# Performance work log

Hardware: AMD Instinct MI355X
Metric: run time of the kernel (lower is better)

The kernel has to match this reference:

```python
import jax, jax.numpy as jnp
import numpy as np

B, HH, WW = 8, 56, 56
N = HH * WW            # 3136 tokens
DIM, NH, SR = 512, 8, 7
HDIM = DIM // 2        # 256
LDIM = DIM - HDIM      # 256
DH = LDIM // NH        # 32
SCALE = DIM ** -0.5
EPS = 1e-5


def _dwconv(x, w):
    # depthwise 3x3, stride 1, SAME (= padding k//2): x [B,C,H,W], w [C,1,3,3]
    return jax.lax.conv_general_dilated(x, w, (1, 1), 'SAME',
                                        feature_group_count=x.shape[1],
                                        dimension_numbers=('NCHW', 'OIHW', 'NCHW'))


def _bn(x, g, b, m, v):
    # inference BatchNorm2d
    s = g * jax.lax.rsqrt(v + EPS)
    return (x - m[None, :, None, None]) * s[None, :, None, None] + b[None, :, None, None]


def _avg_pool(x, k):
    return jax.lax.reduce_window(x, 0.0, jax.lax.add, (1, 1, k, k), (1, 1, k, k), 'VALID') / (k * k)


def _max_pool(x, k):
    return jax.lax.reduce_window(x, -jnp.inf, jax.lax.max, (1, 1, k, k), (1, 1, k, k), 'VALID')


def setup_inputs() -> dict:
    key = jax.random.key(0)
    ks = jax.random.split(key, 32)
    d = {}
    d['x'] = jax.random.normal(ks[0], (B, N, DIM), jnp.float32)
    d['proj_v_w'] = jax.random.normal(ks[1], (LDIM, HDIM), jnp.float32) / np.sqrt(HDIM).astype(np.float32)
    d['conv1_w'] = jax.random.normal(ks[2], (LDIM, 1, 3, 3), jnp.float32) / 3.0
    d['conv2_w'] = jax.random.normal(ks[3], (LDIM, 1, 3, 3), jnp.float32) / 3.0
    d['conv3_w'] = jax.random.normal(ks[4], (HDIM, LDIM, 1, 1), jnp.float32) / np.sqrt(LDIM).astype(np.float32)
    d['conv3_b'] = jax.random.normal(ks[5], (HDIM,), jnp.float32) * 0.1
    d['v_conv_w'] = jax.random.normal(ks[6], (LDIM, 1, 3, 3), jnp.float32) / 3.0
    d['proj_w'] = jax.random.normal(ks[7], (DIM, DIM), jnp.float32) / np.sqrt(DIM).astype(np.float32)
    d['proj_b'] = jax.random.normal(ks[8], (DIM,), jnp.float32) * 0.1
    i = 9
    for pre, c in (('bn1', LDIM), ('bn2', LDIM), ('bn3', HDIM), ('vbn', LDIM)):
        d[pre + '_g'] = jax.random.uniform(ks[i], (c,), jnp.float32, 0.8, 1.2)
        d[pre + '_b'] = jax.random.normal(ks[i + 1], (c,), jnp.float32) * 0.1
        d[pre + '_m'] = jax.random.normal(ks[i + 2], (c,), jnp.float32) * 0.1
        d[pre + '_v'] = jax.random.uniform(ks[i + 3], (c,), jnp.float32, 0.5, 1.5)
        i += 4
    return d


def reference(x, proj_v_w, conv1_w, conv2_w, conv3_w, conv3_b, v_conv_w, proj_w, proj_b,
              bn1_g, bn1_b, bn1_m, bn1_v, bn2_g, bn2_b, bn2_m, bn2_v,
              bn3_g, bn3_b, bn3_m, bn3_v, vbn_g, vbn_b, vbn_m, vbn_v):
    x_high_in = x[..., :HDIM]                       # [B,N,HDIM]
    v = x_high_in @ proj_v_w.T                      # [B,N,LDIM]
    xh = v.reshape(B, HH, WW, LDIM).transpose(0, 3, 1, 2)   # [B,LDIM,H,W]
    xh = _bn(_dwconv(xh, conv1_w), bn1_g, bn1_b, bn1_m, bn1_v)
    q1 = _avg_pool(xh, SR)                          # [B,LDIM,8,8]
    q2 = _max_pool(xh, SR)
    xh = jax.nn.gelu(xh, approximate=False)
    xh = _bn(_dwconv(xh, conv2_w), bn2_g, bn2_b, bn2_m, bn2_v)
    k1 = _avg_pool(xh, SR)
    k2 = _max_pool(xh, SR)
    xh = jax.lax.conv_general_dilated(xh, conv3_w, (1, 1), 'SAME',
                                      dimension_numbers=('NCHW', 'OIHW', 'NCHW')) + conv3_b[None, :, None, None]
    xh = _bn(xh, bn3_g, bn3_b, bn3_m, bn3_v)
    xh = jax.nn.gelu(xh, approximate=False)
    x_high = xh.reshape(B, HDIM, N).transpose(0, 2, 1)      # [B,N,HDIM]

    hq, wq = HH // SR, WW // SR
    nq = hq * wq                                    # 64 pooled tokens

    def heads(t):                                   # [B,LDIM,hq,wq] -> [B,NH,nq,DH]
        return t.reshape(B, NH, DH, nq).transpose(0, 1, 3, 2)

    q = jnp.concatenate([heads(q1), heads(q2)], axis=-1)    # [B,NH,nq,2*DH]
    k = jnp.concatenate([heads(k1), heads(k2)], axis=-1)
    vh = v.reshape(B, N, NH, DH).transpose(0, 2, 1, 3)      # [B,NH,N,DH]

    attn = jnp.einsum('bhqd,bhkd->bhqk', q, k)              # [B,NH,nq,nq]
    attn = attn.reshape(B * NH, nq, hq, wq)
    attn = jax.image.resize(attn, (B * NH, nq, HH, WW), method='bilinear', antialias=False) * SCALE
    attn = attn.reshape(B, NH, nq, N)
    attn = jax.nn.softmax(attn, axis=-1)

    out = jnp.einsum('bhqn,bhnd->bhqd', attn, vh)           # [B,NH,nq,DH]
    out = out.reshape(B, NH, hq, wq, DH).transpose(0, 1, 4, 2, 3).reshape(B, LDIM, hq, wq)
    out = jax.image.resize(out, (B, LDIM, HH, WW), method='bilinear', antialias=False)
    out = _bn(_dwconv(out, v_conv_w), vbn_g, vbn_b, vbn_m, vbn_v)
    x_low = out.reshape(B, LDIM, N).transpose(0, 2, 1)      # [B,N,LDIM]

    y = jnp.concatenate([x_high, x_low], axis=-1) @ proj_w.T + proj_b
    return y
```

## Files before the change

### kernel.cpp

```cpp
#include <hip/hip_runtime.h>
#include <math.h>

#define BB 8
#define HH 56
#define WWD 56
#define NN 3136
#define CC 256
#define DIMM 512
#define NHEAD 8
#define NQ 64
#define EPSF 1e-5f
#define SCALEF 0.04419417382415922f

typedef __attribute__((ext_vector_type(8))) short short8;
typedef __attribute__((ext_vector_type(4))) short short4v;
typedef __attribute__((ext_vector_type(4))) float floatx4;

__device__ __forceinline__ float gelu_f(float x) {
    float z = x * 0.70710678118654752f;
    float a = fabsf(z);
    float t = __builtin_amdgcn_rcpf(1.f + 0.3275911f * a);
    float p = t * (0.254829592f + t * (-0.284496736f + t * (1.421413741f +
              t * (-1.453152027f + t * 1.061405429f))));
    float e = exp2f(-1.44269504f * a * a);
    float erfa = 1.f - p * e;
    float erfz = copysignf(erfa, z);
    return 0.5f * x * (1.f + erfz);
}
__device__ __forceinline__ unsigned short f2bf(float f) {
    union { float f; unsigned u; } v; v.f = f;
    return (unsigned short)((v.u + 0x7fffu + ((v.u >> 16) & 1u)) >> 16);
}
__device__ __forceinline__ float bf2f(unsigned short u) {
    union { unsigned u; float f; } v; v.u = ((unsigned)u) << 16;
    return v.f;
}

__global__ __launch_bounds__(256) void cast3_k(
    const float* __restrict__ a, const float* __restrict__ b,
    const float* __restrict__ cc, unsigned short* __restrict__ da,
    unsigned short* __restrict__ db, unsigned short* __restrict__ dc) {
    int i = blockIdx.x * 256 + threadIdx.x;
    if (i < 65536) {
        da[i] = f2bf(a[i]);
        db[i] = f2bf(b[i]);
    }
    if (i < 262144) dc[i] = f2bf(cc[i]);
}

__global__ __launch_bounds__(256) void gemm_v_mfma(
    const float* __restrict__ x, const unsigned short* __restrict__ w16,
    unsigned short* __restrict__ v16) {
    __shared__ short Ws[128 * 72];
    __shared__ short Xs[128 * 72];
    int n0 = blockIdx.x * 128, c0 = blockIdx.y * 128;
    int tid = threadIdx.x;
    int lane = tid & 63, wv = tid >> 6;
    int wc = wv >> 1, wn = wv & 1;
    int quad = lane >> 4, l16 = lane & 15;
    floatx4 zero = {0.f, 0.f, 0.f, 0.f};
    floatx4 acc[4][4];
#pragma unroll
    for (int ci = 0; ci < 4; ci++)
#pragma unroll
        for (int ni = 0; ni < 4; ni++) acc[ci][ni] = zero;

    for (int k0 = 0; k0 < 256; k0 += 64) {
        {
            int m = tid >> 1;
            int ob = (tid & 1) * 4;
            const float* src = x + (size_t)(n0 + m) * DIMM + k0 + ob * 8;
            short* dst = &Xs[m * 72 + ob * 8];
#pragma unroll
            for (int i2 = 0; i2 < 4; i2++) {
                floatx4 f0 = *(const floatx4*)(src + i2 * 8);
                floatx4 f1 = *(const floatx4*)(src + i2 * 8 + 4);
                short8 pk;
                pk[0] = (short)f2bf(f0[0]); pk[1] = (short)f2bf(f0[1]);
                pk[2] = (short)f2bf(f0[2]); pk[3] = (short)f2bf(f0[3]);
                pk[4] = (short)f2bf(f1[0]); pk[5] = (short)f2bf(f1[1]);
                pk[6] = (short)f2bf(f1[2]); pk[7] = (short)f2bf(f1[3]);
                *(short8*)(dst + i2 * 8) = pk;
            }
        }
#pragma unroll
        for (int i2 = 0; i2 < 4; i2++) {
            int idx = tid + 256 * i2;
            int c = idx >> 3, o = idx & 7;
            *(short8*)&Ws[c * 72 + o * 8] =
                *(const short8*)(const short*)(w16 + (size_t)(c0 + c) * 256 + k0 + o * 8);
        }
        __syncthreads();
#pragma unroll
        for (int kc = 0; kc < 2; kc++) {
            short8 af[4], bf[4];
#pragma unroll
            for (int ci = 0; ci < 4; ci++)
                af[ci] = *(const short8*)&Ws[(wc * 64 + ci * 16 + l16) * 72 + (kc * 4 + quad) * 8];
#pragma unroll
            for (int ni = 0; ni < 4; ni++)
                bf[ni] = *(const short8*)&Xs[(wn * 64 + ni * 16 + l16) * 72 + (kc * 4 + quad) * 8];
#pragma unroll
            for (int ci = 0; ci < 4; ci++)
#pragma unroll
                for (int ni = 0; ni < 4; ni++)
                    acc[ci][ni] = __builtin_amdgcn_mfma_f32_16x16x32_bf16(
                        af[ci], bf[ni], acc[ci][ni], 0, 0, 0);
        }
        __syncthreads();
    }
#pragma unroll
    for (int ni = 0; ni < 4; ni++) {
        int ng = n0 + wn * 64 + ni * 16 + l16;
        int b = ng / NN, n = ng - b * NN;
#pragma unroll
        for (int ci = 0; ci < 4; ci++) {
#pragma unroll
            for (int r = 0; r < 4; r++) {
                int c = c0 + wc * 64 + ci * 16 + quad * 4 + r;
                v16[((size_t)b * CC + c) * NN + n] = f2bf(acc[ci][ni][r]);
            }
        }
    }
}

__device__ __forceinline__ float dw3x3g(const float* __restrict__ Us, int lr,
                                        int x, bool ym, bool yp,
                                        float w0, float w1, float w2, float w3,
                                        float w4, float w5, float w6, float w7,
                                        float w8) {
    bool xm = x > 0, xp = x < 55;
    const float* r1 = &Us[(lr - 1) * 57 + x];
    const float* r2 = &Us[lr * 57 + x];
    const float* r3 = &Us[(lr + 1) * 57 + x];
    float acc = r2[0] * w4;
    if (xm) acc += r2[-1] * w3;
    if (xp) acc += r2[1] * w5;
    if (ym) {
        acc += r1[0] * w1;
        if (xm) acc += r1[-1] * w0;
        if (xp) acc += r1[1] * w2;
    }
    if (yp) {
        acc += r3[0] * w7;
        if (xm) acc += r3[-1] * w6;
        if (xp) acc += r3[1] * w8;
    }
    return acc;
}

__global__ __launch_bounds__(256) void dwconv2x_k(
    const unsigned short* __restrict__ in,
    const float* __restrict__ w1c, const float* __restrict__ g1,
    const float* __restrict__ b1, const float* __restrict__ m1,
    const float* __restrict__ v1,
    const float* __restrict__ w2c, const float* __restrict__ g2,
    const float* __restrict__ b2, const float* __restrict__ m2,
    const float* __restrict__ v2,
    unsigned short* __restrict__ out,
    float* __restrict__ oavg1, float* __restrict__ omax1,
    float* __restrict__ oavg2, float* __restrict__ omax2) {
    __shared__ float Us[18 * 57];
    __shared__ float Cs[16 * 57];
    int bid = blockIdx.x;
    int bc = bid >> 2, chunk = bid & 3;
    int c = bc & 255;
    int r0 = chunk * 14;
    int tid = threadIdx.x;
    const unsigned short* ip = in + (size_t)bc * NN;

    int gl0 = max(r0 - 2, 0), gh0 = min(r0 + 15, 55);
    int nin = (gh0 - gl0 + 1) * 56;
    const unsigned short* ipb = ip + gl0 * 56;
    {
        int e = tid * 4;
        if (e < nin) {
            short4v pk = *(const short4v*)(const short*)(ipb + e);
#pragma unroll
            for (int j = 0; j < 4; j++) {
                int el = e + j;
                int ry = el / 56, x = el - ry * 56;
                int lr = (gl0 + ry) - (r0 - 2);
                Us[lr * 57 + x] = bf2f((unsigned short)pk[j]);
            }
        }
    }
    float w0 = w1c[c * 9 + 0], w1 = w1c[c * 9 + 1], w2 = w1c[c * 9 + 2];
    float w3 = w1c[c * 9 + 3], w4 = w1c[c * 9 + 4], w5 = w1c[c * 9 + 5];
    float w6 = w1c[c * 9 + 6], w7 = w1c[c * 9 + 7], w8 = w1c[c * 9 + 8];
    float s = g1[c] * rsqrtf(v1[c] + EPSF);
    float sh = b1[c] - m1[c] * s;
    __syncthreads();
    int c1lo = max(r0 - 1, 0), c1hi = min(r0 + 14, 55);
    int n1 = (c1hi - c1lo + 1) * 56;
    for (int i = tid; i < n1; i += 256) {
        int ry = i / 56, x = i - ry * 56;
        int gr = c1lo + ry;
        int liu = gr - (r0 - 2);
        float acc = dw3x3g(Us, liu, x, gr > 0, gr < 55,
                           w0, w1, w2, w3, w4, w5, w6, w7, w8);
        Cs[(gr - (r0 - 1)) * 57 + x] = acc * s + sh;
    }
    __syncthreads();
    if (tid < 16) {
        int qy = 2 * chunk + (tid >> 3), qx = tid & 7;
        const float* p0 = &Cs[(qy * 7 - (r0 - 1)) * 57 + qx * 7];
        float sm = 0.f, mx = -INFINITY;
#pragma unroll
        for (int py = 0; py < 7; py++)
#pragma unroll
            for (int px = 0; px < 7; px++) {
                float t = p0[py * 57 + px];
                sm += t;
                mx = fmaxf(mx, t);
            }
        oavg1[(size_t)bc * 64 + qy * 8 + qx] = sm * (1.f / 49.f);
        omax1[(size_t)bc * 64 + qy * 8 + qx] = mx;
    }
    for (int i = tid; i < n1; i += 256) {
        int ry = i / 56, x = i - ry * 56;
        int lr1 = (c1lo + ry) - (r0 - 1);
        Us[lr1 * 57 + x] = gelu_f(Cs[lr1 * 57 + x]);
    }
    w0 = w2c[c * 9 + 0]; w1 = w2c[c * 9 + 1]; w2 = w2c[c * 9 + 2];
    w3 = w2c[c * 9 + 3]; w4 = w2c[c * 9 + 4]; w5 = w2c[c * 9 + 5];
    w6 = w2c[c * 9 + 6]; w7 = w2c[c * 9 + 7]; w8 = w2c[c * 9 + 8];
    s = g2[c] * rsqrtf(v2[c] + EPSF);
    sh = b2[c] - m2[c] * s;
    __syncthreads();
    unsigned short* op = out + (size_t)bc * NN;
    for (int i = tid; i < 14 * 56; i += 256) {
        int ry = i / 56, x = i - ry * 56;
        int gr = r0 + ry;
        int lg = ry + 1;
        float val = dw3x3g(Us, lg, x, gr > 0, gr < 55,
                           w0, w1, w2, w3, w4, w5, w6, w7, w8) * s + sh;
        Cs[ry * 57 + x] = val;
        op[gr * 56 + x] = f2bf(val);
    }
    __syncthreads();
    if (tid < 16) {
        int qy = 2 * chunk + (tid >> 3), qx = tid & 7;
        const float* p0 = &Cs[((qy * 7) - r0) * 57 + qx * 7];
        float sm = 0.f, mx = -INFINITY;
#pragma unroll
        for (int py = 0; py < 7; py++)
#pragma unroll
            for (int px = 0; px < 7; px++) {
                float t = p0[py * 57 + px];
                sm += t;
                mx = fmaxf(mx, t);
            }
        oavg2[(size_t)bc * 64 + qy * 8 + qx] = sm * (1.f / 49.f);
        omax2[(size_t)bc * 64 + qy * 8 + qx] = mx;
    }
}

__global__ __launch_bounds__(256) void conv3_mfma(
    const unsigned short* __restrict__ xin, const unsigned short* __restrict__ w16,
    const float* __restrict__ bias, const float* __restrict__ g,
    const float* __restrict__ bparm, const float* __restrict__ mm,
    const float* __restrict__ vvv, unsigned short* __restrict__ out16) {
    __shared__ short As[128 * 72];
    __shared__ short Bs[128 * 72];
    int m0 = blockIdx.x * 128, c0 = blockIdx.y * 128;
    int tid = threadIdx.x;
    int lane = tid & 63, wv = tid >> 6;
    int wm = wv >> 1, wc = wv & 1;
    int quad = lane >> 4, l16 = lane & 15;
    floatx4 zero = {0.f, 0.f, 0.f, 0.f};
    floatx4 acc[4][4];
#pragma unroll
    for (int mi = 0; mi < 4; mi++)
#pragma unroll
        for (int ci = 0; ci < 4; ci++) acc[mi][ci] = zero;

    for (int k0 = 0; k0 < 256; k0 += 64) {
#pragma unroll
        for (int i2 = 0; i2 < 4; i2++) {
            int mo = i2 * 4 + wv;
            int kk = lane;
            int m8 = m0 + mo * 8;
            int b8 = m8 / NN, n8 = m8 - b8 * NN;
            short8 pk = *(const short8*)(const short*)(
                xin + ((size_t)b8 * CC + (k0 + kk)) * NN + n8);
            short* dst = &As[(mo * 8) * 72 + kk];
#pragma unroll
            for (int j = 0; j < 8; j++) dst[j * 72] = pk[j];
        }
#pragma unroll
        for (int i2 = 0; i2 < 4; i2++) {
            int idx = tid + 256 * i2;
            int c = idx >> 3, o = idx & 7;
            *(short8*)&Bs[c * 72 + o * 8] =
                *(const short8*)(const short*)(w16 + (size_t)(c0 + c) * CC + k0 + o * 8);
        }
        __syncthreads();
#pragma unroll
        for (int kc = 0; kc < 2; kc++) {
            short8 af[4], bf[4];
#pragma unroll
            for (int mi = 0; mi < 4; mi++)
                af[mi] = *(const short8*)&As[(wm * 64 + mi * 16 + l16) * 72 + (kc * 4 + quad) * 8];
#pragma unroll
            for (int ci = 0; ci < 4; ci++)
                bf[ci] = *(const short8*)&Bs[(wc * 64 + ci * 16 + l16) * 72 + (kc * 4 + quad) * 8];
#pragma unroll
            for (int mi = 0; mi < 4; mi++)
#pragma unroll
                for (int ci = 0; ci < 4; ci++)
                    acc[mi][ci] = __builtin_amdgcn_mfma_f32_16x16x32_bf16(
                        af[mi], bf[ci], acc[mi][ci], 0, 0, 0);
        }
        __syncthreads();
    }
#pragma unroll
    for (int ci = 0; ci < 4; ci++) {
        int co = c0 + wc * 64 + ci * 16 + l16;
        float s = g[co] * rsqrtf(vvv[co] + EPSF);
        float sh = bparm[co] - mm[co] * s;
        float bi = bias[co];
#pragma unroll
        for (int mi = 0; mi < 4; mi++) {
            int mbase = m0 + wm * 64 + mi * 16 + quad * 4;
#pragma unroll
            for (int r = 0; r < 4; r++) {
                float val = gelu_f((acc[mi][ci][r] + bi) * s + sh);
                out16[(size_t)(mbase + r) * CC + co] = f2bf(val);
            }
        }
    }
}

__global__ __launch_bounds__(256) void attn_qk_k(
    const float* __restrict__ q1, const float* __restrict__ q2,
    const float* __restrict__ k1, const float* __restrict__ k2,
    float* __restrict__ attn_s) {
    int b = blockIdx.x >> 3, h = blockIdx.x & 7;
    __shared__ float Qs[64][64];
    __shared__ float Ks[64][64];
    int tid = threadIdx.x;
#pragma unroll
    for (int l = 0; l < 16; l++) {
        int e = tid + 256 * l;
        int dt = e >> 6, i = e & 63;
        int d = dt & 31;
        const float* sq = (dt < 32) ? q1 : q2;
        const float* sk = (dt < 32) ? k1 : k2;
        Qs[dt][i] = sq[((size_t)b * CC + h * 32 + d) * NQ + i];
        Ks[dt][i] = sk[((size_t)b * CC + h * 32 + d) * NQ + i];
    }
    __syncthreads();
    int i = tid & 63, jg = tid >> 6;
    float acc[16] = {};
    for (int dt = 0; dt < 64; dt++) {
        float qv = Qs[dt][i];
#pragma unroll
        for (int t = 0; t < 16; t++) acc[t] += qv * Ks[dt][jg * 16 + t];
    }
    float* outp = attn_s + (((size_t)(b * 8 + h) * 64 + i) * 64) + jg * 16;
#pragma unroll
    for (int t = 0; t < 16; t++) outp[t] = acc[t];
}

__global__ __launch_bounds__(256) void attn_pv_k(
    const float* __restrict__ attn_s, const unsigned short* __restrict__ v16,
    float* __restrict__ part_O, float* __restrict__ part_rs) {
    __shared__ float asub[64][68];
    __shared__ float Mq[64];
    __shared__ unsigned short Vs[32][456];
    __shared__ short po4[448][4];
    __shared__ float pw4[448][4];
    int s = blockIdx.x, bh = blockIdx.y;
    int b = bh >> 3, h = bh & 7;
    int tid = threadIdx.x;
    int lane = tid & 63, wv = tid >> 6;
    int quad = lane >> 4, l16 = lane & 15;
    {
        int q = tid & 63, jg = tid >> 6;
        const float* src = attn_s + ((size_t)bh * 64 + q) * 64 + jg * 16;
        float* dst = &asub[q][jg * 16];
#pragma unroll
        for (int t = 0; t < 4; t++) {
            floatx4 f = *(const floatx4*)(src + t * 4);
            f[0] *= SCALEF; f[1] *= SCALEF; f[2] *= SCALEF; f[3] *= SCALEF;
            *(floatx4*)(dst + t * 4) = f;
        }
    }
    {
        int d = tid >> 3, o0 = tid & 7;
        const unsigned short* vp =
            v16 + ((size_t)(b * CC + h * 32 + d)) * NN + s * 448;
#pragma unroll
        for (int t = 0; t < 7; t++) {
            int oc = o0 + t * 8;
            *(short8*)&Vs[d][oc * 8] = *(const short8*)(const short*)(vp + oc * 8);
        }
    }
    for (int idx = tid; idx < 448; idx += 256) {
        int n = s * 448 + idx;
        int oy = n / WWD, ox = n - oy * WWD;
        float sy = (oy + 0.5f) * 0.14285714285714285f - 0.5f;
        float sx = (ox + 0.5f) * 0.14285714285714285f - 0.5f;
        float fy0 = floorf(sy), fx0 = floorf(sx);
        int y0 = (int)fy0, x0 = (int)fx0;
        float fy = sy - fy0, fx = sx - fx0;
        int y0c = max(y0, 0), y1c = min(y0 + 1, 7);
        int x0c = max(x0, 0), x1c = min(x0 + 1, 7);
        po4[idx][0] = (short)(y0c * 8 + x0c);
        po4[idx][1] = (short)(y0c * 8 + x1c);
        po4[idx][2] = (short)(y1c * 8 + x0c);
        po4[idx][3] = (short)(y1c * 8 + x1c);
        pw4[idx][0] = (1.f - fy) * (1.f - fx);
        pw4[idx][1] = (1.f - fy) * fx;
        pw4[idx][2] = fy * (1.f - fx);
        pw4[idx][3] = fy * fx;
    }
    __syncthreads();
    if (tid < 64) {
        float mx = asub[tid][0];
        for (int j = 1; j < 64; j++) mx = fmaxf(mx, asub[tid][j]);
        Mq[tid] = mx;
    }
    __syncthreads();
    int q = wv * 16 + l16;
    float Mv = Mq[q];
    floatx4 zero = {0.f, 0.f, 0.f, 0.f};
    floatx4 acc0 = zero, acc1 = zero;
    float rsum = 0.f;
    for (int cch = 0; cch < 7; cch++) {
#pragma unroll
        for (int kc = 0; kc < 2; kc++) {
            int col = cch * 64 + kc * 32 + quad * 8;
            short8 af;
#pragma unroll
            for (int j = 0; j < 8; j++) {
                int np = col + j;
                float val = pw4[np][0] * asub[q][po4[np][0]]
                          + pw4[np][1] * asub[q][po4[np][1]]
                          + pw4[np][2] * asub[q][po4[np][2]]
                          + pw4[np][3] * asub[q][po4[np][3]];
                float p = exp2f((val - Mv) * 1.44269504f);
                rsum += p;
                af[j] = (short)f2bf(p);
            }
            short8 bf0 = *(const short8*)&Vs[l16][col];
            short8 bf1 = *(const short8*)&Vs[16 + l16][col];
            acc0 = __builtin_amdgcn_mfma_f32_16x16x32_bf16(af, bf0, acc0, 0, 0, 0);
            acc1 = __builtin_amdgcn_mfma_f32_16x16x32_bf16(af, bf1, acc1, 0, 0, 0);
        }
    }
    rsum += __shfl_xor(rsum, 16, 64);
    rsum += __shfl_xor(rsum, 32, 64);
    size_t base = ((size_t)bh * 7 + s) * 64;
    if (lane < 16) part_rs[base + wv * 16 + lane] = rsum;
#pragma unroll
    for (int nt = 0; nt < 2; nt++) {
        floatx4 a = nt ? acc1 : acc0;
#pragma unroll
        for (int r = 0; r < 4; r++) {
            int qo = wv * 16 + quad * 4 + r;
            part_O[(base + qo) * 32 + nt * 16 + l16] = a[r];
        }
    }
}

__global__ __launch_bounds__(256) void upconv_k(
    const float* __restrict__ part_O, const float* __restrict__ part_rs,
    const float* __restrict__ w,
    const float* __restrict__ g, const float* __restrict__ bparm,
    const float* __restrict__ m, const float* __restrict__ v,
    unsigned short* __restrict__ xlow16) {
    __shared__ float ts[64];
    __shared__ float Us[16 * 57];
    int bid = blockIdx.x;
    int bc = bid >> 2, chunk = bid & 3;
    int c = bc & 255;
    int r0 = chunk * 14;
    int tid = threadIdx.x;
    if (tid < 64) {
        int h = c >> 5, d = c & 31;
        int bh = (bc >> 8) * 8 + h;
        float o = 0.f, rs = 0.f;
        for (int s7 = 0; s7 < 7; s7++) {
            size_t base = ((size_t)bh * 7 + s7) * 64 + tid;
            o += part_O[base * 32 + d];
            rs += part_rs[base];
        }
        ts[tid] = o / rs;
    }
    __syncthreads();
    int blo = max(r0 - 1, 0), bhi = min(r0 + 14, 55);
    int nb = (bhi - blo + 1) * 56;
    for (int i = tid; i < nb; i += 256) {
        int ry = i / 56, x = i - ry * 56;
        int gr = blo + ry;
        float sy = (gr + 0.5f) * 0.14285714285714285f - 0.5f;
        float sx = (x + 0.5f) * 0.14285714285714285f - 0.5f;
        float fy0 = floorf(sy), fx0 = floorf(sx);
        int y0 = (int)fy0, x0 = (int)fx0;
        float fy = sy - fy0, fx = sx - fx0;
        int y0c = max(y0, 0), y1c = min(y0 + 1, 7);
        int x0c = max(x0, 0), x1c = min(x0 + 1, 7);
        float v00 = ts[y0c * 8 + x0c], v01 = ts[y0c * 8 + x1c];
        float v10 = ts[y1c * 8 + x0c], v11 = ts[y1c * 8 + x1c];
        Us[(gr - (r0 - 1)) * 57 + x] =
            (1.f - fy) * ((1.f - fx) * v00 + fx * v01) +
            fy * ((1.f - fx) * v10 + fx * v11);
    }
    float w0 = w[c * 9 + 0], w1 = w[c * 9 + 1], w2 = w[c * 9 + 2];
    float w3 = w[c * 9 + 3], w4 = w[c * 9 + 4], w5 = w[c * 9 + 5];
    float w6 = w[c * 9 + 6], w7 = w[c * 9 + 7], w8 = w[c * 9 + 8];
    float s = g[c] * rsqrtf(v[c] + EPSF);
    float sh = bparm[c] - m[c] * s;
    __syncthreads();
    unsigned short* op = xlow16 + (size_t)bc * NN;
    for (int i = tid; i < 14 * 56; i += 256) {
        int ry = i / 56, x = i - ry * 56;
        int gr = r0 + ry;
        float val = dw3x3g(Us, ry + 1, x, gr > 0, gr < 55,
                           w0, w1, w2, w3, w4, w5, w6, w7, w8);
        op[gr * 56 + x] = f2bf(val * s + sh);
    }
}

__global__ __launch_bounds__(256) void proj_mfma(
    const unsigned short* __restrict__ xh16, const unsigned short* __restrict__ xl16,
    const unsigned short* __restrict__ w16, const float* __restrict__ bias,
    float* __restrict__ y) {
    __shared__ short As[128 * 72];
    __shared__ short Bs[128 * 72];
    int m0 = blockIdx.x * 128, c0 = blockIdx.y * 128;
    int tid = threadIdx.x;
    int lane = tid & 63, wv = tid >> 6;
    int wm = wv >> 1, wc = wv & 1;
    int quad = lane >> 4, l16 = lane & 15;
    floatx4 zero = {0.f, 0.f, 0.f, 0.f};
    floatx4 acc[4][4];
#pragma unroll
    for (int mi = 0; mi < 4; mi++)
#pragma unroll
        for (int ci = 0; ci < 4; ci++) acc[mi][ci] = zero;

    for (int k0 = 0; k0 < 512; k0 += 64) {
        if (k0 < 256) {
#pragma unroll
            for (int i2 = 0; i2 < 4; i2++) {
                int idx = tid + 256 * i2;
                int m = idx >> 3, o = idx & 7;
                *(short8*)&As[m * 72 + o * 8] =
                    *(const short8*)(const short*)(xh16 + (size_t)(m0 + m) * CC + k0 + o * 8);
            }
        } else {
#pragma unroll
            for (int i2 = 0; i2 < 4; i2++) {
                int mo = i2 * 4 + wv;
                int kk = lane;
                int m8 = m0 + mo * 8;
                int b8 = m8 / NN, n8 = m8 - b8 * NN;
                short8 pk = *(const short8*)(const short*)(
                    xl16 + ((size_t)b8 * CC + (k0 - 256 + kk)) * NN + n8);
                short* dst = &As[(mo * 8) * 72 + kk];
#pragma unroll
                for (int j = 0; j < 8; j++) dst[j * 72] = pk[j];
            }
        }
#pragma unroll
        for (int i2 = 0; i2 < 4; i2++) {
            int idx = tid + 256 * i2;
            int c = idx >> 3, o = idx & 7;
            *(short8*)&Bs[c * 72 + o * 8] =
                *(const short8*)(const short*)(w16 + (size_t)(c0 + c) * DIMM + k0 + o * 8);
        }
        __syncthreads();
#pragma unroll
        for (int kc = 0; kc < 2; kc++) {
            short8 af[4], bf[4];
#pragma unroll
            for (int mi = 0; mi < 4; mi++)
                af[mi] = *(const short8*)&As[(wm * 64 + mi * 16 + l16) * 72 + (kc * 4 + quad) * 8];
#pragma unroll
            for (int ci = 0; ci < 4; ci++)
                bf[ci] = *(const short8*)&Bs[(wc * 64 + ci * 16 + l16) * 72 + (kc * 4 + quad) * 8];
#pragma unroll
            for (int mi = 0; mi < 4; mi++)
#pragma unroll
                for (int ci = 0; ci < 4; ci++)
                    acc[mi][ci] = __builtin_amdgcn_mfma_f32_16x16x32_bf16(
                        af[mi], bf[ci], acc[mi][ci], 0, 0, 0);
        }
        __syncthreads();
    }
#pragma unroll
    for (int mi = 0; mi < 4; mi++) {
        int mbase = m0 + wm * 64 + mi * 16 + quad * 4;
#pragma unroll
        for (int ci = 0; ci < 4; ci++) {
            int co = c0 + wc * 64 + ci * 16 + l16;
            float bi = bias[co];
#pragma unroll
            for (int r = 0; r < 4; r++)
                y[(size_t)(mbase + r) * DIMM + co] = acc[mi][ci][r] + bi;
        }
    }
}

extern "C" void kernel_launch(void* const* d_in, const int* in_sizes, int n_in,
                              void* d_out, int out_size, void* d_ws, size_t ws_size,
                              hipStream_t stream) {
    const float* x        = (const float*)d_in[0];
    const float* proj_v_w = (const float*)d_in[1];
    const float* conv1_w  = (const float*)d_in[2];
    const float* conv2_w  = (const float*)d_in[3];
    const float* conv3_w  = (const float*)d_in[4];
    const float* conv3_b  = (const float*)d_in[5];
    const float* v_conv_w = (const float*)d_in[6];
    const float* proj_w   = (const float*)d_in[7];
    const float* proj_b   = (const float*)d_in[8];
    const float* bn1_g = (const float*)d_in[9],  *bn1_b = (const float*)d_in[10];
    const float* bn1_m = (const float*)d_in[11], *bn1_v = (const float*)d_in[12];
    const float* bn2_g = (const float*)d_in[13], *bn2_b = (const float*)d_in[14];
    const float* bn2_m = (const float*)d_in[15], *bn2_v = (const float*)d_in[16];
    const float* bn3_g = (const float*)d_in[17], *bn3_b = (const float*)d_in[18];
    const float* bn3_m = (const float*)d_in[19], *bn3_v = (const float*)d_in[20];
    const float* vbn_g = (const float*)d_in[21], *vbn_b = (const float*)d_in[22];
    const float* vbn_m = (const float*)d_in[23], *vbn_v = (const float*)d_in[24];

    const size_t big = (size_t)BB * CC * NN;
    unsigned short* v16    = (unsigned short*)d_ws;
    unsigned short* bufA16 = v16 + big;
    unsigned short* bufB16 = bufA16 + big;
    unsigned short* xh16   = bufB16 + big;
    unsigned short* xlow16 = xh16 + big;
    float* small = (float*)(xlow16 + big);
    float* q1 = small;
    float* q2 = q1 + (size_t)BB * CC * NQ;
    float* k1 = q2 + (size_t)BB * CC * NQ;
    float* k2 = k1 + (size_t)BB * CC * NQ;
    float* attn_s = k2 + (size_t)BB * CC * NQ;
    float* out_s  = attn_s + (size_t)BB * NHEAD * NQ * NQ;
    float* part_O = out_s + (size_t)BB * CC * NQ;
    float* part_rs = part_O + (size_t)64 * 7 * 64 * 32;
    unsigned short* w16v  = (unsigned short*)(part_rs + 64 * 7 * 64);
    unsigned short* w16c3 = w16v + 65536;
    unsigned short* w16p  = w16c3 + 65536;

    cast3_k<<<1024, 256, 0, stream>>>(proj_v_w, conv3_w, proj_w, w16v, w16c3, w16p);

    gemm_v_mfma<<<dim3(196, 2), 256, 0, stream>>>(x, w16v, v16);
    dwconv2x_k<<<BB * CC * 4, 256, 0, stream>>>(
        v16, conv1_w, bn1_g, bn1_b, bn1_m, bn1_v,
        conv2_w, bn2_g, bn2_b, bn2_m, bn2_v, bufB16, q1, q2, k1, k2);
    conv3_mfma<<<dim3(196, 2), 256, 0, stream>>>(bufB16, w16c3, conv3_b,
                                                 bn3_g, bn3_b, bn3_m, bn3_v, xh16);
    attn_qk_k<<<64, 256, 0, stream>>>(q1, q2, k1, k2, attn_s);
    attn_pv_k<<<dim3(7, 64), 256, 0, stream>>>(attn_s, v16, part_O, part_rs);
    upconv_k<<<BB * CC * 4, 256, 0, stream>>>(part_O, part_rs, v_conv_w,
                                              vbn_g, vbn_b, vbn_m, vbn_v, xlow16);
    proj_mfma<<<dim3(196, 4), 256, 0, stream>>>(xh16, xlow16, w16p, proj_b, (float*)d_out);
}
```

Before: 265.9 us.

## Fuse weight bf16 casts into GEMMs, precompute softmax row max in QK kernel

Removes the separate weight-cast kernel by converting fp32 weights to bf16 while staging each GEMM tile in shared memory. Swaps the grid axes so blocks sharing the same token tile run next to each other, which should improve reuse of the activation tile in L2. Moves the attention scaling and per-row max into the QK kernel so the PV kernel skips a serial max loop and one barrier. The trade-off is that every GEMM block now re-reads and re-converts fp32 weights, doubling weight traffic per tile.

After: 303.4 us. 1.14x slower.

```diff
diff --git a/kernel.cpp b/kernel.cpp
--- a/kernel.cpp
+++ b/kernel.cpp
@@ -36,24 +36,32 @@
     return v.f;
 }
 
-__global__ __launch_bounds__(256) void cast3_k(
-    const float* __restrict__ a, const float* __restrict__ b,
-    const float* __restrict__ cc, unsigned short* __restrict__ da,
-    unsigned short* __restrict__ db, unsigned short* __restrict__ dc) {
-    int i = blockIdx.x * 256 + threadIdx.x;
-    if (i < 65536) {
-        da[i] = f2bf(a[i]);
-        db[i] = f2bf(b[i]);
-    }
-    if (i < 262144) dc[i] = f2bf(cc[i]);
+__device__ __forceinline__ void stage_w_f32(const float* __restrict__ wsrc,
+                                            int rowlen, int c0, int k0,
+                                            short* __restrict__ Bs, int tid) {
+    int c = tid >> 1;
+    int ob = (tid & 1) * 4;
+    const float* src = wsrc + (size_t)(c0 + c) * rowlen + k0 + ob * 8;
+    short* dst = &Bs[c * 72 + ob * 8];
+#pragma unroll
+    for (int i2 = 0; i2 < 4; i2++) {
+        floatx4 f0 = *(const floatx4*)(src + i2 * 8);
+        floatx4 f1 = *(const floatx4*)(src + i2 * 8 + 4);
+        short8 pk;
+        pk[0] = (short)f2bf(f0[0]); pk[1] = (short)f2bf(f0[1]);
+        pk[2] = (short)f2bf(f0[2]); pk[3] = (short)f2bf(f0[3]);
+        pk[4] = (short)f2bf(f1[0]); pk[5] = (short)f2bf(f1[1]);
+        pk[6] = (short)f2bf(f1[2]); pk[7] = (short)f2bf(f1[3]);
+        *(short8*)(dst + i2 * 8) = pk;
+    }
 }
 
 __global__ __launch_bounds__(256) void gemm_v_mfma(
-    const float* __restrict__ x, const unsigned short* __restrict__ w16,
+    const float* __restrict__ x, const float* __restrict__ wsrc,
     unsigned short* __restrict__ v16) {
     __shared__ short Ws[128 * 72];
     __shared__ short Xs[128 * 72];
-    int n0 = blockIdx.x * 128, c0 = blockIdx.y * 128;
+    int n0 = blockIdx.y * 128, c0 = blockIdx.x * 128;
     int tid = threadIdx.x;
     int lane = tid & 63, wv = tid >> 6;
     int wc = wv >> 1, wn = wv & 1;
@@ -83,13 +91,7 @@
                 *(short8*)(dst + i2 * 8) = pk;
             }
         }
-#pragma unroll
-        for (int i2 = 0; i2 < 4; i2++) {
-            int idx = tid + 256 * i2;
-            int c = idx >> 3, o = idx & 7;
-            *(short8*)&Ws[c * 72 + o * 8] =
-                *(const short8*)(const short*)(w16 + (size_t)(c0 + c) * 256 + k0 + o * 8);
-        }
+        stage_w_f32(wsrc, 256, c0, k0, Ws, tid);
         __syncthreads();
 #pragma unroll
         for (int kc = 0; kc < 2; kc++) {
@@ -257,13 +259,13 @@
 }
 
 __global__ __launch_bounds__(256) void conv3_mfma(
-    const unsigned short* __restrict__ xin, const unsigned short* __restrict__ w16,
+    const unsigned short* __restrict__ xin, const float* __restrict__ wsrc,
     const float* __restrict__ bias, const float* __restrict__ g,
     const float* __restrict__ bparm, const float* __restrict__ mm,
     const float* __restrict__ vvv, unsigned short* __restrict__ out16) {
     __shared__ short As[128 * 72];
     __shared__ short Bs[128 * 72];
-    int m0 = blockIdx.x * 128, c0 = blockIdx.y * 128;
+    int m0 = blockIdx.y * 128, c0 = blockIdx.x * 128;
     int tid = threadIdx.x;
     int lane = tid & 63, wv = tid >> 6;
     int wm = wv >> 1, wc = wv & 1;
@@ -288,13 +290,7 @@
 #pragma unroll
             for (int j = 0; j < 8; j++) dst[j * 72] = pk[j];
         }
-#pragma unroll
-        for (int i2 = 0; i2 < 4; i2++) {
-            int idx = tid + 256 * i2;
-            int c = idx >> 3, o = idx & 7;
-            *(short8*)&Bs[c * 72 + o * 8] =
-                *(const short8*)(const short*)(w16 + (size_t)(c0 + c) * CC + k0 + o * 8);
-        }
+        stage_w_f32(wsrc, CC, c0, k0, Bs, tid);
         __syncthreads();
 #pragma unroll
         for (int kc = 0; kc < 2; kc++) {
@@ -335,10 +331,11 @@
 __global__ __launch_bounds__(256) void attn_qk_k(
     const float* __restrict__ q1, const float* __restrict__ q2,
     const float* __restrict__ k1, const float* __restrict__ k2,
-    float* __restrict__ attn_s) {
+    float* __restrict__ attn_s, float* __restrict__ mq) {
     int b = blockIdx.x >> 3, h = blockIdx.x & 7;
     __shared__ float Qs[64][64];
     __shared__ float Ks[64][64];
+    __shared__ float pm[4][64];
     int tid = threadIdx.x;
 #pragma unroll
     for (int l = 0; l < 16; l++) {
@@ -358,16 +355,29 @@
 #pragma unroll
         for (int t = 0; t < 16; t++) acc[t] += qv * Ks[dt][jg * 16 + t];
     }
+    float mx = -INFINITY;
+#pragma unroll
+    for (int t = 0; t < 16; t++) {
+        acc[t] *= SCALEF;
+        mx = fmaxf(mx, acc[t]);
+    }
+    pm[jg][i] = mx;
     float* outp = attn_s + (((size_t)(b * 8 + h) * 64 + i) * 64) + jg * 16;
 #pragma unroll
     for (int t = 0; t < 16; t++) outp[t] = acc[t];
+    __syncthreads();
+    if (tid < 64) {
+        float m = fmaxf(fmaxf(pm[0][tid], pm[1][tid]),
+                        fmaxf(pm[2][tid], pm[3][tid]));
+        mq[(size_t)(b * 8 + h) * 64 + tid] = m;
+    }
 }
 
 __global__ __launch_bounds__(256) void attn_pv_k(
-    const float* __restrict__ attn_s, const unsigned short* __restrict__ v16,
+    const float* __restrict__ attn_s, const float* __restrict__ mq,
+    const unsigned short* __restrict__ v16,
     float* __restrict__ part_O, float* __restrict__ part_rs) {
     __shared__ float asub[64][68];
-    __shared__ float Mq[64];
     __shared__ unsigned short Vs[32][456];
     __shared__ short po4[448][4];
     __shared__ float pw4[448][4];
@@ -376,16 +386,15 @@
     int tid = threadIdx.x;
     int lane = tid & 63, wv = tid >> 6;
     int quad = lane >> 4, l16 = lane & 15;
+    int q = wv * 16 + l16;
+    float Mv = mq[(size_t)bh * 64 + q];
     {
-        int q = tid & 63, jg = tid >> 6;
-        const float* src = attn_s + ((size_t)bh * 64 + q) * 64 + jg * 16;
-        float* dst = &asub[q][jg * 16];
-#pragma unroll
-        for (int t = 0; t < 4; t++) {
-            floatx4 f = *(const floatx4*)(src + t * 4);
-            f[0] *= SCALEF; f[1] *= SCALEF; f[2] *= SCALEF; f[3] *= SCALEF;
-            *(floatx4*)(dst + t * 4) = f;
-        }
+        int qq = tid & 63, jg = tid >> 6;
+        const float* src = attn_s + ((size_t)bh * 64 + qq) * 64 + jg * 16;
+        float* dst = &asub[qq][jg * 16];
+#pragma unroll
+        for (int t = 0; t < 4; t++)
+            *(floatx4*)(dst + t * 4) = *(const floatx4*)(src + t * 4);
     }
     {
         int d = tid >> 3, o0 = tid & 7;
@@ -417,14 +426,6 @@
         pw4[idx][3] = fy * fx;
     }
     __syncthreads();
-    if (tid < 64) {
-        float mx = asub[tid][0];
-        for (int j = 1; j < 64; j++) mx = fmaxf(mx, asub[tid][j]);
-        Mq[tid] = mx;
-    }
-    __syncthreads();
-    int q = wv * 16 + l16;
-    float Mv = Mq[q];
     floatx4 zero = {0.f, 0.f, 0.f, 0.f};
     floatx4 acc0 = zero, acc1 = zero;
     float rsum = 0.f;
@@ -526,11 +527,11 @@
 
 __global__ __launch_bounds__(256) void proj_mfma(
     const unsigned short* __restrict__ xh16, const unsigned short* __restrict__ xl16,
-    const unsigned short* __restrict__ w16, const float* __restrict__ bias,
+    const float* __restrict__ wsrc, const float* __restrict__ bias,
     float* __restrict__ y) {
     __shared__ short As[128 * 72];
     __shared__ short Bs[128 * 72];
-    int m0 = blockIdx.x * 128, c0 = blockIdx.y * 128;
+    int m0 = blockIdx.y * 128, c0 = blockIdx.x * 128;
     int tid = threadIdx.x;
     int lane = tid & 63, wv = tid >> 6;
     int wm = wv >> 1, wc = wv & 1;
@@ -565,13 +566,7 @@
                 for (int j = 0; j < 8; j++) dst[j * 72] = pk[j];
             }
         }
-#pragma unroll
-        for (int i2 = 0; i2 < 4; i2++) {
-            int idx = tid + 256 * i2;
-            int c = idx >> 3, o = idx & 7;
-            *(short8*)&Bs[c * 72 + o * 8] =
-                *(const short8*)(const short*)(w16 + (size_t)(c0 + c) * DIMM + k0 + o * 8);
-        }
+        stage_w_f32(wsrc, DIMM, c0, k0, Bs, tid);
         __syncthreads();
 #pragma unroll
         for (int kc = 0; kc < 2; kc++) {
@@ -641,21 +636,18 @@
     float* out_s  = attn_s + (size_t)BB * NHEAD * NQ * NQ;
     float* part_O = out_s + (size_t)BB * CC * NQ;
     float* part_rs = part_O + (size_t)64 * 7 * 64 * 32;
-    unsigned short* w16v  = (unsigned short*)(part_rs + 64 * 7 * 64);
-    unsigned short* w16c3 = w16v + 65536;
-    unsigned short* w16p  = w16c3 + 65536;
-
-    cast3_k<<<1024, 256, 0, stream>>>(proj_v_w, conv3_w, proj_w, w16v, w16c3, w16p);
-
-    gemm_v_mfma<<<dim3(196, 2), 256, 0, stream>>>(x, w16v, v16);
+    float* mq = part_rs + (size_t)64 * 7 * 64;
+
+    gemm_v_mfma<<<dim3(2, 196), 256, 0, stream>>>(x, proj_v_w, v16);
     dwconv2x_k<<<BB * CC * 4, 256, 0, stream>>>(
         v16, conv1_w, bn1_g, bn1_b, bn1_m, bn1_v,
         conv2_w, bn2_g, bn2_b, bn2_m, bn2_v, bufB16, q1, q2, k1, k2);
-    conv3_mfma<<<dim3(196, 2), 256, 0, stream>>>(bufB16, w16c3, conv3_b,
+    conv3_mfma<<<dim3(2, 196), 256, 0, stream>>>(bufB16, conv3_w, conv3_b,
                                                  bn3_g, bn3_b, bn3_m, bn3_v, xh16);
-    attn_qk_k<<<64, 256, 0, stream>>>(q1, q2, k1, k2, attn_s);
-    attn_pv_k<<<dim3(7, 64), 256, 0, stream>>>(attn_s, v16, part_O, part_rs);
+    attn_qk_k<<<64, 256, 0, stream>>>(q1, q2, k1, k2, attn_s, mq);
+    attn_pv_k<<<dim3(7, 64), 256, 0, stream>>>(attn_s, mq, v16, part_O, part_rs);
     upconv_k<<<BB * CC * 4, 256, 0, stream>>>(part_O, part_rs, v_conv_w,
                                               vbn_g, vbn_b, vbn_m, vbn_v, xlow16);
-    proj_mfma<<<dim3(196, 4), 256, 0, stream>>>(xh16, xlow16, w16p, proj_b, (float*)d_out);
-}
+    proj_mfma<<<dim3(4, 196), 256, 0, stream>>>(xh16, xlow16, proj_w, proj_b,
+                                                (float*)d_out);
+}
```
